# Kernel optimization log

Measured on AMD Instinct MI355X. Metric: run time of the kernel, lower is better.

## Reference

```python
import jax, jax.numpy as jnp
import numpy as np

B, S, D, H = 2, 2048, 1024, 16
HD = D // H  # head_dim = 64


def setup_inputs() -> dict:
    key = jax.random.key(0)
    ks = jax.random.split(key, 6)
    scale = 0.02
    x = jax.random.normal(ks[0], (B, S, D), dtype=jnp.float32)
    Wq = jax.random.normal(ks[1], (D, D), dtype=jnp.float32) * scale
    Wk = jax.random.normal(ks[2], (D, D), dtype=jnp.float32) * scale
    Wv = jax.random.normal(ks[3], (D, D), dtype=jnp.float32) * scale
    Wo = jax.random.normal(ks[4], (D, D), dtype=jnp.float32) * scale
    bo = jnp.zeros((D,), dtype=jnp.float32)
    return {"x": x, "Wq": Wq, "Wk": Wk, "Wv": Wv, "Wo": Wo, "bo": bo}


def reference(x, Wq, Wk, Wv, Wo, bo):
    b, s, _ = x.shape
    # Linear projections (qkv_bias=False), split into heads: [b, h, s, hd]
    def split_heads(t):
        return t.reshape(b, s, H, HD).transpose(0, 2, 1, 3)
    q = split_heads(x @ Wq)
    k = split_heads(x @ Wk)
    v = split_heads(x @ Wv)
    # Scaled dot-product scores: [b, h, s, s]
    scores = jnp.einsum('bhqd,bhkd->bhqk', q, k) / jnp.sqrt(jnp.float32(HD))
    # Causal mask: triu(ones, diagonal=1) positions -> -inf
    causal = jnp.triu(jnp.ones((s, s), dtype=bool), k=1)
    scores = jnp.where(causal, -jnp.inf, scores)
    attn = jax.nn.softmax(scores, axis=-1)
    # dropout p=0.0 (eval-equivalent): identity
    ctx = jnp.einsum('bhqk,bhkd->bhqd', attn, v)  # [b, h, s, hd]
    ctx = ctx.transpose(0, 2, 1, 3).reshape(b, s, D)
    return ctx @ Wo + bo
```

## Files before the change

kernel.cpp:

```cpp
#include <hip/hip_runtime.h>
#include <math.h>

#define BB 2
#define SS 2048
#define DD 1024
#define HH 16
#define HD 64
#define MM (BB * SS)

typedef __bf16 bf16;
typedef __attribute__((ext_vector_type(8))) __bf16 bf16x8;
typedef __attribute__((ext_vector_type(4))) __bf16 bf16x4;
typedef __attribute__((ext_vector_type(4))) short short4v;
typedef __attribute__((ext_vector_type(4))) float f32x4;

#if __has_builtin(__builtin_amdgcn_exp2f)
#define EXP2F(x) __builtin_amdgcn_exp2f(x)
#else
#define EXP2F(x) exp2f(x)
#endif

__device__ __forceinline__ f32x4 pv_mfma16(bf16x4 a, short4v b, f32x4 c) {
    return __builtin_amdgcn_mfma_f32_16x16x16bf16_1k(
        __builtin_bit_cast(short4v, a), b, c, 0, 0, 0);
}

__device__ __forceinline__ void gld_lds16(const void* g, void* l) {
    __builtin_amdgcn_global_load_lds(
        (const __attribute__((address_space(1))) void*)g,
        (__attribute__((address_space(3))) void*)l, 16, 0, 0);
}

__global__ __launch_bounds__(256) void prep(
    const float* __restrict__ x,
    const float* __restrict__ W0, const float* __restrict__ W1,
    const float* __restrict__ W2, const float* __restrict__ W3,
    bf16* __restrict__ xb, bf16* __restrict__ Wt)
{
    __shared__ float tile[32][33];
    const int z = blockIdx.z;
    if (z < 4) {
        const float* W = (z == 0) ? W0 : (z == 1) ? W1 : (z == 2) ? W2 : W3;
        bf16* O = Wt + (size_t)z * DD * DD;
        const int tx = threadIdx.x & 31, ty = threadIdx.x >> 5;
        const int k0 = blockIdx.y * 32, n0 = blockIdx.x * 32;
#pragma unroll
        for (int i = 0; i < 4; ++i)
            tile[ty + i * 8][tx] = W[(size_t)(k0 + ty + i * 8) * DD + n0 + tx];
        __syncthreads();
#pragma unroll
        for (int i = 0; i < 4; ++i)
            O[(size_t)(n0 + ty + i * 8) * DD + k0 + tx] = (bf16)tile[tx][ty + i * 8];
    } else {
        const int lb = (z - 4) * 1024 + blockIdx.y * 32 + blockIdx.x;
        const size_t i = ((size_t)lb * 256 + threadIdx.x) * 8;
        const float4 a = *(const float4*)(x + i);
        const float4 b = *(const float4*)(x + i + 4);
        bf16x8 o;
        o[0] = (bf16)a.x; o[1] = (bf16)a.y; o[2] = (bf16)a.z; o[3] = (bf16)a.w;
        o[4] = (bf16)b.x; o[5] = (bf16)b.y; o[6] = (bf16)b.z; o[7] = (bf16)b.w;
        *(bf16x8*)(xb + i) = o;
    }
}

template <int SWAP>
__device__ __forceinline__ void mfma_core(
    const bf16* __restrict__ A, const bf16* __restrict__ Bt,
    int bm, int bn, int K, bf16* As, bf16* Bs, f32x4 (&acc)[4][4])
{
    const int t = threadIdx.x;
    const int w = t >> 6;
    const int l16 = t & 15, quad = (t >> 4) & 3;
    const int wr = w >> 1, wc = w & 1;
    const int arow = t >> 2;
    const int achk = (((t & 3) ^ ((t >> 3) & 3)) << 3);

    const bf16* gA = A + (size_t)(bm + arow) * K + achk;
    const bf16* gB = Bt + (size_t)(bn + arow) * K + achk;
    bf16* lA = As + w * 512;
    bf16* lB = Bs + w * 512;

    const int swz = (l16 >> 1) & 3;
    int offA[4], offB[4];
#pragma unroll
    for (int i = 0; i < 4; ++i) {
        offA[i] = (wr * 64 + i * 16 + l16) * 32 + ((quad ^ swz) << 3);
        offB[i] = (wc * 64 + i * 16 + l16) * 32 + ((quad ^ swz) << 3);
    }

#define GSTAGE(BUF, KO) do {                                                  \
        gld_lds16(gA + (KO),                  lA + (BUF) * 4096);             \
        gld_lds16(gA + (size_t)64 * K + (KO), lA + (BUF) * 4096 + 2048);      \
        gld_lds16(gB + (KO),                  lB + (BUF) * 4096);             \
        gld_lds16(gB + (size_t)64 * K + (KO), lB + (BUF) * 4096 + 2048);      \
    } while (0)

#define GCOMPUTE(BUF) do {                                                    \
        const bf16* Ab = As + (BUF) * 4096;                                   \
        const bf16* Bb = Bs + (BUF) * 4096;                                   \
        bf16x8 af[4], bv[4];                                                  \
        _Pragma("unroll")                                                     \
        for (int i = 0; i < 4; ++i) {                                         \
            af[i] = *(const bf16x8*)(Ab + offA[i]);                           \
            bv[i] = *(const bf16x8*)(Bb + offB[i]);                           \
        }                                                                     \
        _Pragma("unroll")                                                     \
        for (int mi = 0; mi < 4; ++mi)                                        \
            _Pragma("unroll")                                                 \
            for (int ni = 0; ni < 4; ++ni)                                    \
                acc[mi][ni] = SWAP                                            \
                    ? __builtin_amdgcn_mfma_f32_16x16x32_bf16(                \
                          bv[ni], af[mi], acc[mi][ni], 0, 0, 0)               \
                    : __builtin_amdgcn_mfma_f32_16x16x32_bf16(                \
                          af[mi], bv[ni], acc[mi][ni], 0, 0, 0);              \
    } while (0)

#define GBAR() do {                                                           \
        asm volatile("s_barrier" ::: "memory");                               \
        __builtin_amdgcn_sched_barrier(0);                                    \
    } while (0)

    GSTAGE(0, 0);
    const int nk = K >> 5;
    for (int kt = 0; kt < nk; kt += 2) {
        GSTAGE(1, (kt + 1) << 5);
        asm volatile("s_waitcnt vmcnt(4)" ::: "memory");
        GBAR();
        GCOMPUTE(0);
        asm volatile("s_waitcnt lgkmcnt(0)" ::: "memory");
        GBAR();
        if (kt + 2 < nk) {
            GSTAGE(0, (kt + 2) << 5);
            asm volatile("s_waitcnt vmcnt(4)" ::: "memory");
        } else {
            asm volatile("s_waitcnt vmcnt(0)" ::: "memory");
        }
        GBAR();
        GCOMPUTE(1);
        asm volatile("s_waitcnt lgkmcnt(0)" ::: "memory");
        GBAR();
    }
#undef GBAR
#undef GCOMPUTE
#undef GSTAGE
}

__global__ __launch_bounds__(256) void gemm_qkv(
    const bf16* __restrict__ xb, const bf16* __restrict__ Wt,
    bf16* __restrict__ Qb, bf16* __restrict__ Kb, bf16* __restrict__ Vb)
{
    __shared__ __align__(16) bf16 As[2 * 128 * 32];
    __shared__ __align__(16) bf16 Bs[2 * 128 * 32];
    const int bm = blockIdx.y * 128, bn = blockIdx.x * 128, z = blockIdx.z;

    const int t = threadIdx.x;
    const int w = t >> 6, l16 = t & 15, quad = (t >> 4) & 3;
    const int wr = w >> 1, wc = w & 1;

    f32x4 acc[4][4] = {};
    if (z < 2) {
        mfma_core<1>(xb, Wt + (size_t)z * DD * DD, bm, bn, DD, As, Bs, acc);
        bf16* outp = (z == 0) ? Qb : Kb;
        const float scl = (z == 0) ? 0.18033688011f : 1.0f;
#pragma unroll
        for (int mi = 0; mi < 4; ++mi) {
            const int srow = bm + wr * 64 + mi * 16 + l16;
            const int b = srow >> 11, s = srow & (SS - 1);
#pragma unroll
            for (int ni = 0; ni < 4; ++ni) {
                const int colb = bn + wc * 64 + ni * 16 + quad * 4;
                const int h = colb >> 6, hd = colb & 63;
                bf16x4 o;
#pragma unroll
                for (int r = 0; r < 4; ++r) o[r] = (bf16)(acc[mi][ni][r] * scl);
                *(bf16x4*)(outp + ((size_t)((b * HH + h) * SS + s)) * HD + hd) = o;
            }
        }
    } else {
        mfma_core<0>(xb, Wt + (size_t)2 * DD * DD, bm, bn, DD, As, Bs, acc);
#pragma unroll
        for (int mi = 0; mi < 4; ++mi) {
            const int srow0 = bm + wr * 64 + mi * 16 + quad * 4;
            const int b = srow0 >> 11, s0 = srow0 & (SS - 1);
#pragma unroll
            for (int ni = 0; ni < 4; ++ni) {
                const int col = bn + wc * 64 + ni * 16 + l16;
                const int h = col >> 6, hd = col & 63;
                bf16x4 o;
#pragma unroll
                for (int r = 0; r < 4; ++r) o[r] = (bf16)acc[mi][ni][r];
                *(bf16x4*)(Vb + ((size_t)((b * HH + h) * HD + hd)) * SS + s0) = o;
            }
        }
    }
}

__global__ __launch_bounds__(256) void gemm_out(
    const bf16* __restrict__ ctx, const bf16* __restrict__ Wto,
    const float* __restrict__ bias, float* __restrict__ out)
{
    __shared__ __align__(16) bf16 As[2 * 128 * 32];
    __shared__ __align__(16) bf16 Bs[2 * 128 * 32];
    const int bm = blockIdx.y * 128, bn = blockIdx.x * 128;

    f32x4 acc[4][4] = {};
    mfma_core<1>(ctx, Wto, bm, bn, DD, As, Bs, acc);

    const int t = threadIdx.x;
    const int w = t >> 6, l16 = t & 15, quad = (t >> 4) & 3;
    const int wr = w >> 1, wc = w & 1;

#pragma unroll
    for (int mi = 0; mi < 4; ++mi) {
        const int row = bm + wr * 64 + mi * 16 + l16;
#pragma unroll
        for (int ni = 0; ni < 4; ++ni) {
            const int colb = bn + wc * 64 + ni * 16 + quad * 4;
            const float4 b4 = *(const float4*)(bias + colb);
            float4 o;
            o.x = acc[mi][ni][0] + b4.x;
            o.y = acc[mi][ni][1] + b4.y;
            o.z = acc[mi][ni][2] + b4.z;
            o.w = acc[mi][ni][3] + b4.w;
            *(float4*)(out + (size_t)row * DD + colb) = o;
        }
    }
}

__global__ __launch_bounds__(256, 4) void attn_flash(
    const bf16* __restrict__ Q, const bf16* __restrict__ K,
    const bf16* __restrict__ Vt, bf16* __restrict__ ctx)
{
    __shared__ __align__(16) bf16 Ks[2][64 * 64];
    __shared__ __align__(16) bf16 Vs[2][64 * 64];

    const int t = threadIdx.x;
    const int w = t >> 6;
    const int lane = t & 63;
    const int l16 = lane & 15, quad = lane >> 4;

    const int L  = blockIdx.x;
    const int bh = L & 31;
    const int idx = L >> 5;
    const int pg = idx >> 3, pr = idx & 7;
    const int qg = (pg == 0) ? 31 - pr : (pg == 1) ? pr
                 : (pg == 2) ? 23 - pr : 8 + pr;
    const int q0b = qg * 64;
    const int q0w = q0b + w * 16;
    const int qrow = q0w + l16;
    const int nkt = qg + 1;

    const bf16* Qp = Q  + ((size_t)bh * SS + q0w) * HD;
    const bf16* Kp = K  + (size_t)bh * SS * HD;
    const bf16* Vp = Vt + (size_t)bh * HD * SS;

    const bf16x8 bQ0 = *(const bf16x8*)(Qp + l16 * HD + quad * 8);
    const bf16x8 bQ1 = *(const bf16x8*)(Qp + l16 * HD + 32 + quad * 8);

    const int r8 = lane >> 3, cs = lane & 7;
    const int rowA = (w * 2) * 8 + r8, rowB = (w * 2 + 1) * 8 + r8;
    const int cA = (cs - rowA) & 7, cB = (cs - rowB) & 7;
    const bf16* gK0 = Kp + (size_t)rowA * HD + cA * 8;
    const bf16* gK1 = Kp + (size_t)rowB * HD + cB * 8;
    const bf16* gV0 = Vp + (size_t)rowA * SS + cA * 8;
    const bf16* gV1 = Vp + (size_t)rowB * SS + cB * 8;
    bf16* const lK0 = &Ks[0][(w * 2) * 512];
    bf16* const lK1 = &Ks[0][(w * 2 + 1) * 512];
    bf16* const lV0 = &Vs[0][(w * 2) * 512];
    bf16* const lV1 = &Vs[0][(w * 2 + 1) * 512];

#define STAGE(BUF, KB) do {                                              \
        gld_lds16(gK0 + (size_t)(KB) * HD, lK0 + (BUF) * 4096);          \
        gld_lds16(gK1 + (size_t)(KB) * HD, lK1 + (BUF) * 4096);          \
        gld_lds16(gV0 + (KB),              lV0 + (BUF) * 4096);          \
        gld_lds16(gV1 + (KB),              lV1 + (BUF) * 4096);          \
    } while (0)

    const int offK0 = l16 * 64 + ((quad + l16) & 7) * 8;
    const int offK1 = l16 * 64 + ((quad + 4 + l16) & 7) * 8;
    int offV[4];
#pragma unroll
    for (int mi = 0; mi < 4; ++mi)
        offV[mi] = l16 * 64 + ((((quad >> 1) + 2 * mi + l16) & 7) * 8)
                 + (quad & 1) * 4;

    const bf16* const KsB = &Ks[0][0];
    const bf16* const VsB = &Vs[0][0];

    f32x4 accO[4] = {{0,0,0,0},{0,0,0,0},{0,0,0,0},{0,0,0,0}};
    float Lr = 0.f;

#define TILE(BUF, KB) do {                                                   \
        f32x4 St[4] = {{0,0,0,0},{0,0,0,0},{0,0,0,0},{0,0,0,0}};             \
        _Pragma("unroll")                                                    \
        for (int mi = 0; mi < 4; ++mi) {                                     \
            const bf16x8 a0 = *(const bf16x8*)(KsB + (BUF) * 4096            \
                                               + mi * 1024 + offK0);         \
            const bf16x8 a1 = *(const bf16x8*)(KsB + (BUF) * 4096            \
                                               + mi * 1024 + offK1);         \
            St[mi] = __builtin_amdgcn_mfma_f32_16x16x32_bf16(                \
                a0, bQ0, St[mi], 0, 0, 0);                                   \
            St[mi] = __builtin_amdgcn_mfma_f32_16x16x32_bf16(                \
                a1, bQ1, St[mi], 0, 0, 0);                                   \
        }                                                                    \
        if ((KB) + 63 > q0w) {                                               \
            _Pragma("unroll")                                                \
            for (int mi = 0; mi < 4; ++mi)                                   \
                _Pragma("unroll")                                            \
                for (int rr = 0; rr < 4; ++rr)                               \
                    if ((KB) + mi * 16 + quad * 4 + rr > qrow)               \
                        St[mi][rr] = -1e30f;                                 \
        }                                                                    \
        float rs = 0.f;                                                      \
        short4v pb[4];                                                       \
        _Pragma("unroll")                                                    \
        for (int mi = 0; mi < 4; ++mi) {                                     \
            bf16x4 pk;                                                       \
            _Pragma("unroll")                                                \
            for (int rr = 0; rr < 4; ++rr) {                                 \
                const float p = EXP2F(St[mi][rr]);                           \
                rs += p;                                                     \
                pk[rr] = (bf16)p;                                            \
            }                                                                \
            pb[mi] = __builtin_bit_cast(short4v, pk);                        \
        }                                                                    \
        rs += __shfl_xor(rs, 16);                                            \
        rs += __shfl_xor(rs, 32);                                            \
        Lr += rs;                                                            \
        _Pragma("unroll")                                                    \
        for (int mi = 0; mi < 4; ++mi) {                                     \
            _Pragma("unroll")                                                 \
            for (int db = 0; db < 4; ++db) {                                 \
                const bf16x4 aV = *(const bf16x4*)(VsB + (BUF) * 4096        \
                                                   + db * 1024 + offV[mi]);  \
                accO[db] = pv_mfma16(aV, pb[mi], accO[db]);                  \
            }                                                                \
        }                                                                    \
    } while (0)

    STAGE(0, 0);
    int kb = 0;
    for (int kt = 0; kt + 2 <= nkt; kt += 2) {
        __syncthreads();
        STAGE(1, kb + 64);
        TILE(0, kb);
        __syncthreads();
        if (kt + 2 < nkt) STAGE(0, kb + 128);
        TILE(1, kb + 64);
        kb += 128;
    }
    if (nkt & 1) {
        __syncthreads();
        TILE(0, kb);
    }
#undef TILE
#undef STAGE

    const float rinv = 1.0f / Lr;
    const int b = bh >> 4, h = bh & (HH - 1);
    bf16* op = ctx + ((size_t)(b * SS + q0w + l16)) * DD + h * HD;
#pragma unroll
    for (int db = 0; db < 4; ++db) {
        bf16x4 o;
#pragma unroll
        for (int rr = 0; rr < 4; ++rr) o[rr] = (bf16)(accO[db][rr] * rinv);
        *(bf16x4*)(op + db * 16 + quad * 4) = o;
    }
}

extern "C" void kernel_launch(void* const* d_in, const int* in_sizes, int n_in,
                              void* d_out, int out_size, void* d_ws, size_t ws_size,
                              hipStream_t stream)
{
    const float* x  = (const float*)d_in[0];
    const float* Wq = (const float*)d_in[1];
    const float* Wk = (const float*)d_in[2];
    const float* Wv = (const float*)d_in[3];
    const float* Wo = (const float*)d_in[4];
    const float* bo = (const float*)d_in[5];
    float* out = (float*)d_out;

    const size_t chunk = (size_t)MM * DD;
    bf16* xb  = (bf16*)d_ws;
    bf16* Wt  = xb + chunk;
    bf16* Qb  = Wt + 4 * (size_t)DD * DD;
    bf16* Kb  = Qb + chunk;
    bf16* Vb  = Kb + chunk;
    bf16* ctx = Vb + chunk;

    prep<<<dim3(32, 32, 6), dim3(256), 0, stream>>>(x, Wq, Wk, Wv, Wo, xb, Wt);

    gemm_qkv<<<dim3(DD / 128, MM / 128, 3), dim3(256), 0, stream>>>(xb, Wt, Qb, Kb, Vb);

    attn_flash<<<dim3(BB * HH * (SS / 64)), dim3(256), 0, stream>>>(Qb, Kb, Vb, ctx);

    gemm_out<<<dim3(DD / 128, MM / 128), dim3(256), 0, stream>>>(
        ctx, Wt + 3 * (size_t)DD * DD, bo, out);
}
```

Measured before the change: 179.0 us.

## Use 128-row query blocks with 8 waves sharing each staged K/V tile

The attention kernel now runs 512 threads per block covering 128 query rows instead of 64, so each staged 64-key K/V tile in shared memory is reused by twice as many waves. This halves the total K/V global-to-LDS traffic and the block count. Each thread now issues one load per tensor per stage, and the last diagonal tile is processed only by the upper four waves. The cost is coarser scheduling granularity, fewer blocks for load balance, and per-block occupancy constraints from the 512-thread launch bound.

```diff
diff --git a/kernel.cpp b/kernel.cpp
--- a/kernel.cpp
+++ b/kernel.cpp
@@ -227,7 +227,7 @@
     }
 }
 
-__global__ __launch_bounds__(256, 4) void attn_flash(
+__global__ __launch_bounds__(512, 4) void attn_flash(
     const bf16* __restrict__ Q, const bf16* __restrict__ K,
     const bf16* __restrict__ Vt, bf16* __restrict__ ctx)
 {
@@ -241,14 +241,12 @@
 
     const int L  = blockIdx.x;
     const int bh = L & 31;
-    const int idx = L >> 5;
-    const int pg = idx >> 3, pr = idx & 7;
-    const int qg = (pg == 0) ? 31 - pr : (pg == 1) ? pr
-                 : (pg == 2) ? 23 - pr : 8 + pr;
-    const int q0b = qg * 64;
+    const int slot = L >> 5;
+    const int g = (slot < 8) ? 15 - slot : slot - 8;
+    const int q0b = g * 128;
     const int q0w = q0b + w * 16;
     const int qrow = q0w + l16;
-    const int nkt = qg + 1;
+    const int nkt = 2 * g + 2;
 
     const bf16* Qp = Q  + ((size_t)bh * SS + q0w) * HD;
     const bf16* Kp = K  + (size_t)bh * SS * HD;
@@ -257,23 +255,16 @@
     const bf16x8 bQ0 = *(const bf16x8*)(Qp + l16 * HD + quad * 8);
     const bf16x8 bQ1 = *(const bf16x8*)(Qp + l16 * HD + 32 + quad * 8);
 
-    const int r8 = lane >> 3, cs = lane & 7;
-    const int rowA = (w * 2) * 8 + r8, rowB = (w * 2 + 1) * 8 + r8;
-    const int cA = (cs - rowA) & 7, cB = (cs - rowB) & 7;
-    const bf16* gK0 = Kp + (size_t)rowA * HD + cA * 8;
-    const bf16* gK1 = Kp + (size_t)rowB * HD + cB * 8;
-    const bf16* gV0 = Vp + (size_t)rowA * SS + cA * 8;
-    const bf16* gV1 = Vp + (size_t)rowB * SS + cB * 8;
-    bf16* const lK0 = &Ks[0][(w * 2) * 512];
-    bf16* const lK1 = &Ks[0][(w * 2 + 1) * 512];
-    bf16* const lV0 = &Vs[0][(w * 2) * 512];
-    bf16* const lV1 = &Vs[0][(w * 2 + 1) * 512];
+    const int srow = w * 8 + (lane >> 3);
+    const int c = ((lane & 7) - srow) & 7;
+    const bf16* gK = Kp + (size_t)srow * HD + c * 8;
+    const bf16* gV = Vp + (size_t)srow * SS + c * 8;
+    bf16* const lK = &Ks[0][w * 512];
+    bf16* const lV = &Vs[0][w * 512];
 
 #define STAGE(BUF, KB) do {                                              \
-        gld_lds16(gK0 + (size_t)(KB) * HD, lK0 + (BUF) * 4096);          \
-        gld_lds16(gK1 + (size_t)(KB) * HD, lK1 + (BUF) * 4096);          \
-        gld_lds16(gV0 + (KB),              lV0 + (BUF) * 4096);          \
-        gld_lds16(gV1 + (KB),              lV1 + (BUF) * 4096);          \
+        gld_lds16(gK + (size_t)(KB) * HD, lK + (BUF) * 4096);            \
+        gld_lds16(gV + (KB),              lV + (BUF) * 4096);            \
     } while (0)
 
     const int offK0 = l16 * 64 + ((quad + l16) & 7) * 8;
@@ -340,18 +331,18 @@
 
     STAGE(0, 0);
     int kb = 0;
-    for (int kt = 0; kt + 2 <= nkt; kt += 2) {
+    for (int kt = 0; kt < nkt; kt += 2) {
         __syncthreads();
         STAGE(1, kb + 64);
         TILE(0, kb);
         __syncthreads();
-        if (kt + 2 < nkt) STAGE(0, kb + 128);
-        TILE(1, kb + 64);
+        if (kt + 2 < nkt) {
+            STAGE(0, kb + 128);
+            TILE(1, kb + 64);
+        } else {
+            if (w >= 4) TILE(1, kb + 64);
+        }
         kb += 128;
-    }
-    if (nkt & 1) {
-        __syncthreads();
-        TILE(0, kb);
     }
 #undef TILE
 #undef STAGE
@@ -392,7 +383,7 @@
 
     gemm_qkv<<<dim3(DD / 128, MM / 128, 3), dim3(256), 0, stream>>>(xb, Wt, Qb, Kb, Vb);
 
-    attn_flash<<<dim3(BB * HH * (SS / 64)), dim3(256), 0, stream>>>(Qb, Kb, Vb, ctx);
+    attn_flash<<<dim3(BB * HH * (SS / 128)), dim3(512), 0, stream>>>(Qb, Kb, Vb, ctx);
 
     gemm_out<<<dim3(DD / 128, MM / 128), dim3(256), 0, stream>>>(
         ctx, Wt + 3 * (size_t)DD * DD, bo, out);
```

Result: no change. 178.0 us (median of 3 runs) (-0.6%).
